# Kernel optimization log

Measured on AMD Instinct MI355X. Metric: run time of the kernel, lower is better.

The kernel has to match this reference:

```python
import jax, jax.numpy as jnp
import numpy as np

NORMALIZED_LENGTH = 512  # init kwarg
T_FRAMES = 32768
N_LM = 543  # mediapipe holistic landmark count


def setup_inputs() -> dict:
    key = jax.random.key(0)
    kf, kn, kd, ki = jax.random.split(key, 4)
    frames = jax.random.uniform(kf, (T_FRAMES, N_LM, 3), dtype=jnp.float32)
    nan_mask = jax.random.uniform(kn, (T_FRAMES, N_LM, 3)) < 0.10
    frames = jnp.where(nan_mask, jnp.float32(jnp.nan), frames)
    drop = jax.random.uniform(kd, (T_FRAMES,)) < 0.05
    hand_zone = jnp.arange(N_LM) >= 468
    frames = jnp.where(drop[:, None, None] & hand_zone[None, :, None], jnp.float32(jnp.nan), frames)
    lips_idx = jax.random.randint(ki, (40,), 0, 468, dtype=jnp.int32)
    return {"frames": frames, "lips_idx": lips_idx}


def _nan_mean0(x):
    # tf_nan_mean over axis 0 (keepdims); 0/0 -> NaN in TF is immediately zeroed
    # afterwards, so we emit 0 directly (identical forward values, safe grads).
    finite = ~jnp.isnan(x)
    s = jnp.where(finite, x, jnp.zeros((), x.dtype)).sum(axis=0, keepdims=True)
    c = finite.sum(axis=0, keepdims=True)
    return jnp.where(c == 0, jnp.zeros((), x.dtype), s / jnp.maximum(c, 1).astype(x.dtype))


def reference(frames, lips_idx):
    fr = frames[:, :, :2]                       # drop z coord
    lh = fr[:, 468:489]                         # [T, 21, 2]
    rh = fr[:, 522:543]                         # [T, 21, 2]
    lh = jnp.stack([lh[..., 0], 1.0 - lh[..., 1]], axis=-1)
    rh = jnp.stack([1.0 - rh[..., 0], 1.0 - rh[..., 1]], axis=-1)
    # stack hands, NaN->0, sum over the 2-hand axis
    hand = jnp.nan_to_num(lh) + jnp.nan_to_num(rh)   # [T, 21, 2]
    keep = hand.sum(axis=(1, 2)) != 0.0              # frames with >=1 visible hand
    hand = hand[keep]                                # [S, 21, 2]
    lips = fr[:, lips_idx][keep]                     # [S, 40, 2]
    lips = jnp.where(jnp.isnan(lips), _nan_mean0(lips), lips)
    raw = jnp.concatenate([hand, lips], axis=1)      # [S, 61, 2]
    S = int(raw.shape[0])
    # tf.linspace(0, S-1, L+1) cast to int32 -> segment boundaries (truncation)
    b = np.linspace(0.0, S - 1.0, NORMALIZED_LENGTH + 1).astype(np.int32)
    # frame t belongs to bin i with b[i] <= t < b[i+1]; t >= b[L] maps to L (dropped)
    seg = jnp.asarray(np.searchsorted(b, np.arange(S), side="right") - 1)
    sums = jax.ops.segment_sum(raw, seg, num_segments=NORMALIZED_LENGTH)
    cnt = jax.ops.segment_sum(jnp.ones((S,), raw.dtype), seg, num_segments=NORMALIZED_LENGTH)
    # raw is NaN-free at this point, so nan-mean == plain mean; empty bin -> NaN -> 0
    mean = jnp.where(cnt[:, None, None] == 0, jnp.zeros((), raw.dtype),
                     sums / jnp.maximum(cnt, 1.0)[:, None, None])
    sampled = mean.reshape(NORMALIZED_LENGTH, -1)    # Flatten -> [L, 122]
    rows = sampled.sum(axis=1) != 0.0                # drop all-zero (empty) bins
    return sampled[rows]
```

## Files before the change

kernel.cpp:

```cpp
#include <hip/hip_runtime.h>

#define T_FRAMES 32768
#define ROWF 1629
#define NSEG 512
#define NVAL 122
#define STRIDE 128
#define PADI 16

__global__ __launch_bounds__(1024) void k1_keep_stats(
    const float* __restrict__ frames, const int* __restrict__ lips_idx,
    int* __restrict__ keep, float* __restrict__ lip_sum,
    int* __restrict__ lip_cnt, float* __restrict__ stage) {
  __shared__ float ls[80];
  __shared__ int lc[80];
  int tid = threadIdx.x;
  if (tid < 80) { ls[tid] = 0.0f; lc[tid] = 0; }
  __syncthreads();

  int lane = tid & 63;
  int wid = tid >> 6;
  int t = blockIdx.x * 16 + wid;
  const float* f = frames + (size_t)t * ROWF;
  float* srow = stage + (size_t)t * STRIDE;

  float hv = 0.0f;
  if (lane < 42) {
    int j = lane >> 1, c = lane & 1;
    float lh = f[(468 + j) * 3 + c];
    float rh = f[(522 + j) * 3 + c];
    float a = (c == 0) ? lh : (1.0f - lh);
    float b = 1.0f - rh;
    a = (a == a) ? a : 0.0f;
    b = (b == b) ? b : 0.0f;
    hv = a + b;
    srow[lane] = hv;
  }
  float s = hv;
  #pragma unroll
  for (int off = 32; off > 0; off >>= 1) s += __shfl_down(s, off);
  s = __shfl(s, 0);
  int kp = (s != 0.0f) ? 1 : 0;
  if (lane == 0) keep[t] = kp;

  #pragma unroll
  for (int p = 0; p < 2; ++p) {
    int v = lane + p * 64;
    if (v < 80) {
      int j = v >> 1, c = v & 1;
      float x = f[lips_idx[j] * 3 + c];
      srow[42 + v] = x;
      if (kp && (x == x)) {
        atomicAdd(&ls[v], x);
        atomicAdd(&lc[v], 1);
      }
    }
  }
  __syncthreads();
  if (tid < 80) {
    atomicAdd(&lip_sum[tid * PADI], ls[tid]);
    atomicAdd(&lip_cnt[tid * PADI], lc[tid]);
  }
}

__global__ __launch_bounds__(1024) void k2_scan(const int* __restrict__ keep,
                                                int* __restrict__ kept_t,
                                                int* __restrict__ Sp) {
  __shared__ int wsum[16];
  int tid = threadIdx.x;
  const int PER = T_FRAMES / 1024;
  int base = tid * PER;
  int fl[PER];
  int local = 0;
  #pragma unroll
  for (int k = 0; k < PER; ++k) { fl[k] = keep[base + k]; local += fl[k]; }

  int lane = tid & 63, wid = tid >> 6;
  int scan = local;
  #pragma unroll
  for (int off = 1; off < 64; off <<= 1) {
    int n = __shfl_up(scan, off);
    if (lane >= off) scan += n;
  }
  if (lane == 63) wsum[wid] = scan;
  __syncthreads();
  if (tid < 16) {
    int v = wsum[tid];
    #pragma unroll
    for (int off = 1; off < 16; off <<= 1) {
      int n = __shfl_up(v, off);
      if (tid >= off) v += n;
    }
    wsum[tid] = v;
  }
  __syncthreads();
  int excl = ((wid == 0) ? 0 : wsum[wid - 1]) + (scan - local);
  #pragma unroll
  for (int k = 0; k < PER; ++k) {
    if (fl[k]) kept_t[excl++] = base + k;
  }
  if (tid == 1023) Sp[0] = wsum[15];
}

__global__ __launch_bounds__(512) void k3_segments(
    const float* __restrict__ stage, const int* __restrict__ kept_t,
    const int* __restrict__ Sp, const float* __restrict__ lip_sum,
    const int* __restrict__ lip_cnt, float* __restrict__ out, int out_size) {
  __shared__ int seglist[128];
  __shared__ float part[4][128];
  int tid = threadIdx.x;
  int v = tid & 127;
  int r = tid >> 7;
  int seg = blockIdx.x;
  long long Sm1 = (long long)Sp[0] - 1;
  if (Sm1 < 0) Sm1 = 0;
  int lo = (int)(((long long)seg * Sm1) >> 9);
  int hi = (int)(((long long)(seg + 1) * Sm1) >> 9);
  int cnt = hi - lo;

  for (int k = tid; k < cnt; k += 512) seglist[k] = kept_t[lo + k];
  __syncthreads();

  float cm = 0.0f;
  if (v >= 42 && v < NVAL) {
    int w = v - 42;
    int c = lip_cnt[w * PADI];
    cm = (c == 0) ? 0.0f : lip_sum[w * PADI] / (float)c;
  }

  float acc = 0.0f;
  if (v < NVAL) {
    for (int k = r; k < cnt; k += 4) {
      float x = stage[(size_t)seglist[k] * STRIDE + v];
      acc += (x == x) ? x : cm;
    }
  }
  part[r][v] = acc;
  __syncthreads();
  if (r == 0 && v < NVAL) {
    float tot = part[0][v] + part[1][v] + part[2][v] + part[3][v];
    float mean = (cnt == 0) ? 0.0f : tot / (float)cnt;
    int o = seg * NVAL + v;
    if (o < out_size) out[o] = mean;
  }
}

extern "C" void kernel_launch(void* const* d_in, const int* in_sizes, int n_in,
                              void* d_out, int out_size, void* d_ws, size_t ws_size,
                              hipStream_t stream) {
  const float* frames = (const float*)d_in[0];
  const int* lips_idx = (const int*)d_in[1];
  float* out = (float*)d_out;

  char* ws = (char*)d_ws;
  int* keep      = (int*)(ws);
  int* kept_t    = (int*)(ws + 131072);
  int* Sp        = (int*)(ws + 262144);
  float* lip_sum = (float*)(ws + 262208);
  int* lip_cnt   = (int*)(ws + 267328);
  float* stage   = (float*)(ws + 274432);

  hipMemsetAsync((void*)lip_sum, 0, 10240, stream);

  k1_keep_stats<<<2048, 1024, 0, stream>>>(frames, lips_idx, keep, lip_sum,
                                           lip_cnt, stage);
  k2_scan<<<1, 1024, 0, stream>>>(keep, kept_t, Sp);
  k3_segments<<<NSEG, 512, 0, stream>>>(stage, kept_t, Sp, lip_sum, lip_cnt,
                                        out, out_size);
}
```

Baseline: 320.4 us.

## Fuse compaction scan into stats kernel via last-block pattern; skip dropped frames

```diff
diff --git a/kernel.cpp b/kernel.cpp
--- a/kernel.cpp
+++ b/kernel.cpp
@@ -6,20 +6,25 @@
 #define NVAL 122
 #define STRIDE 128
 #define PADI 16
+#define K1_BLOCKS 2048
 
-__global__ __launch_bounds__(1024) void k1_keep_stats(
+__global__ __launch_bounds__(1024) void k1_fused(
     const float* __restrict__ frames, const int* __restrict__ lips_idx,
     int* __restrict__ keep, float* __restrict__ lip_sum,
-    int* __restrict__ lip_cnt, float* __restrict__ stage) {
+    int* __restrict__ lip_cnt, float* __restrict__ stage,
+    int* __restrict__ counter, int* __restrict__ kept_t,
+    int* __restrict__ Sp) {
   __shared__ float ls[80];
   __shared__ int lc[80];
+  __shared__ int wsum[16];
+  __shared__ int isLast;
   int tid = threadIdx.x;
   if (tid < 80) { ls[tid] = 0.0f; lc[tid] = 0; }
   __syncthreads();
 
   int lane = tid & 63;
-  int wid = tid >> 6;
-  int t = blockIdx.x * 16 + wid;
+  int wv = tid >> 6;
+  int t = blockIdx.x * 16 + wv;
   const float* f = frames + (size_t)t * ROWF;
   float* srow = stage + (size_t)t * STRIDE;
 
@@ -33,7 +38,6 @@
     a = (a == a) ? a : 0.0f;
     b = (b == b) ? b : 0.0f;
     hv = a + b;
-    srow[lane] = hv;
   }
   float s = hv;
   #pragma unroll
@@ -42,16 +46,19 @@
   int kp = (s != 0.0f) ? 1 : 0;
   if (lane == 0) keep[t] = kp;
 
-  #pragma unroll
-  for (int p = 0; p < 2; ++p) {
-    int v = lane + p * 64;
-    if (v < 80) {
-      int j = v >> 1, c = v & 1;
-      float x = f[lips_idx[j] * 3 + c];
-      srow[42 + v] = x;
-      if (kp && (x == x)) {
-        atomicAdd(&ls[v], x);
-        atomicAdd(&lc[v], 1);
+  if (kp) {
+    if (lane < 42) srow[lane] = hv;
+    #pragma unroll
+    for (int p = 0; p < 2; ++p) {
+      int v = lane + p * 64;
+      if (v < 80) {
+        int j = v >> 1, c = v & 1;
+        float x = f[lips_idx[j] * 3 + c];
+        srow[42 + v] = x;
+        if (x == x) {
+          atomicAdd(&ls[v], x);
+          atomicAdd(&lc[v], 1);
+        }
       }
     }
   }
@@ -60,28 +67,30 @@
     atomicAdd(&lip_sum[tid * PADI], ls[tid]);
     atomicAdd(&lip_cnt[tid * PADI], lc[tid]);
   }
-}
 
-__global__ __launch_bounds__(1024) void k2_scan(const int* __restrict__ keep,
-                                                int* __restrict__ kept_t,
-                                                int* __restrict__ Sp) {
-  __shared__ int wsum[16];
-  int tid = threadIdx.x;
+  __syncthreads();
+  if (tid == 0) {
+    __threadfence();
+    int prev = atomicAdd(counter, 1);
+    isLast = (prev == K1_BLOCKS - 1) ? 1 : 0;
+  }
+  __syncthreads();
+  if (!isLast) return;
+  __threadfence();
+
   const int PER = T_FRAMES / 1024;
   int base = tid * PER;
-  int fl[PER];
   int local = 0;
-  #pragma unroll
-  for (int k = 0; k < PER; ++k) { fl[k] = keep[base + k]; local += fl[k]; }
+  #pragma unroll 8
+  for (int k = 0; k < PER; ++k) local += keep[base + k];
 
-  int lane = tid & 63, wid = tid >> 6;
   int scan = local;
   #pragma unroll
   for (int off = 1; off < 64; off <<= 1) {
     int n = __shfl_up(scan, off);
     if (lane >= off) scan += n;
   }
-  if (lane == 63) wsum[wid] = scan;
+  if (lane == 63) wsum[wv] = scan;
   __syncthreads();
   if (tid < 16) {
     int v = wsum[tid];
@@ -93,10 +102,9 @@
     wsum[tid] = v;
   }
   __syncthreads();
-  int excl = ((wid == 0) ? 0 : wsum[wid - 1]) + (scan - local);
-  #pragma unroll
+  int excl = ((wv == 0) ? 0 : wsum[wv - 1]) + (scan - local);
   for (int k = 0; k < PER; ++k) {
-    if (fl[k]) kept_t[excl++] = base + k;
+    if (keep[base + k]) kept_t[excl++] = base + k;
   }
   if (tid == 1023) Sp[0] = wsum[15];
 }
@@ -155,15 +163,15 @@
   int* keep      = (int*)(ws);
   int* kept_t    = (int*)(ws + 131072);
   int* Sp        = (int*)(ws + 262144);
+  int* counter   = (int*)(ws + 262144 + 4);
   float* lip_sum = (float*)(ws + 262208);
   int* lip_cnt   = (int*)(ws + 267328);
   float* stage   = (float*)(ws + 274432);
 
-  hipMemsetAsync((void*)lip_sum, 0, 10240, stream);
+  hipMemsetAsync((void*)(ws + 262144), 0, 12288, stream);
 
-  k1_keep_stats<<<2048, 1024, 0, stream>>>(frames, lips_idx, keep, lip_sum,
-                                           lip_cnt, stage);
-  k2_scan<<<1, 1024, 0, stream>>>(keep, kept_t, Sp);
+  k1_fused<<<K1_BLOCKS, 1024, 0, stream>>>(frames, lips_idx, keep, lip_sum,
+                                           lip_cnt, stage, counter, kept_t, Sp);
   k3_segments<<<NSEG, 512, 0, stream>>>(stage, kept_t, Sp, lip_sum, lip_cnt,
                                         out, out_size);
 }
```

Result: slower. 427.6 us (+33.5%).

## Stage frame groups into LDS with vector loads and replace global atomics with partials

Applied to the files above, without the earlier changes.

```diff
diff --git a/kernel.cpp b/kernel.cpp
--- a/kernel.cpp
+++ b/kernel.cpp
@@ -5,68 +5,97 @@
 #define NSEG 512
 #define NVAL 122
 #define STRIDE 128
-#define PADI 16
+#define G 8
+#define NBLK (T_FRAMES / G)
 
-__global__ __launch_bounds__(1024) void k1_keep_stats(
+__global__ __launch_bounds__(1024) void k1_stream(
     const float* __restrict__ frames, const int* __restrict__ lips_idx,
-    int* __restrict__ keep, float* __restrict__ lip_sum,
-    int* __restrict__ lip_cnt, float* __restrict__ stage) {
+    int* __restrict__ keep, float* __restrict__ psum, int* __restrict__ pcnt,
+    float* __restrict__ stage) {
+  __shared__ float buf[G * ROWF];
   __shared__ float ls[80];
   __shared__ int lc[80];
+  __shared__ int idx3[40];
   int tid = threadIdx.x;
   if (tid < 80) { ls[tid] = 0.0f; lc[tid] = 0; }
+  if (tid < 40) idx3[tid] = lips_idx[tid] * 3;
+
+  const float4* src = (const float4*)(frames + (size_t)blockIdx.x * (G * ROWF));
+  float4* dst = (float4*)buf;
+  #pragma unroll
+  for (int i = tid; i < (G * ROWF) / 4; i += 1024) dst[i] = src[i];
   __syncthreads();
 
   int lane = tid & 63;
-  int wid = tid >> 6;
-  int t = blockIdx.x * 16 + wid;
-  const float* f = frames + (size_t)t * ROWF;
-  float* srow = stage + (size_t)t * STRIDE;
+  int wv = tid >> 6;
+  if (wv < G) {
+    const float* fb = buf + wv * ROWF;
+    int t = blockIdx.x * G + wv;
+    float* srow = stage + (size_t)t * STRIDE;
 
-  float hv = 0.0f;
-  if (lane < 42) {
-    int j = lane >> 1, c = lane & 1;
-    float lh = f[(468 + j) * 3 + c];
-    float rh = f[(522 + j) * 3 + c];
-    float a = (c == 0) ? lh : (1.0f - lh);
-    float b = 1.0f - rh;
-    a = (a == a) ? a : 0.0f;
-    b = (b == b) ? b : 0.0f;
-    hv = a + b;
-    srow[lane] = hv;
-  }
-  float s = hv;
-  #pragma unroll
-  for (int off = 32; off > 0; off >>= 1) s += __shfl_down(s, off);
-  s = __shfl(s, 0);
-  int kp = (s != 0.0f) ? 1 : 0;
-  if (lane == 0) keep[t] = kp;
+    float hv = 0.0f;
+    if (lane < 42) {
+      int j = lane >> 1, c = lane & 1;
+      float lh = fb[1404 + 3 * j + c];
+      float rh = fb[1566 + 3 * j + c];
+      float a = (c == 0) ? lh : (1.0f - lh);
+      float b = 1.0f - rh;
+      a = (a == a) ? a : 0.0f;
+      b = (b == b) ? b : 0.0f;
+      hv = a + b;
+      srow[lane] = hv;
+    }
+    float s = hv;
+    #pragma unroll
+    for (int off = 32; off > 0; off >>= 1) s += __shfl_down(s, off);
+    s = __shfl(s, 0);
+    int kp = (s != 0.0f) ? 1 : 0;
+    if (lane == 0) keep[t] = kp;
 
-  #pragma unroll
-  for (int p = 0; p < 2; ++p) {
-    int v = lane + p * 64;
-    if (v < 80) {
-      int j = v >> 1, c = v & 1;
-      float x = f[lips_idx[j] * 3 + c];
-      srow[42 + v] = x;
-      if (kp && (x == x)) {
-        atomicAdd(&ls[v], x);
-        atomicAdd(&lc[v], 1);
+    #pragma unroll
+    for (int p = 0; p < 2; ++p) {
+      int v = lane + p * 64;
+      if (v < 80) {
+        int j = v >> 1, c = v & 1;
+        float x = fb[idx3[j] + c];
+        srow[42 + v] = x;
+        if (kp && (x == x)) {
+          atomicAdd(&ls[v], x);
+          atomicAdd(&lc[v], 1);
+        }
       }
     }
   }
   __syncthreads();
   if (tid < 80) {
-    atomicAdd(&lip_sum[tid * PADI], ls[tid]);
-    atomicAdd(&lip_cnt[tid * PADI], lc[tid]);
+    psum[(size_t)tid * NBLK + blockIdx.x] = ls[tid];
+    pcnt[(size_t)tid * NBLK + blockIdx.x] = lc[tid];
   }
 }
 
-__global__ __launch_bounds__(1024) void k2_scan(const int* __restrict__ keep,
-                                                int* __restrict__ kept_t,
-                                                int* __restrict__ Sp) {
+__global__ __launch_bounds__(1024) void k2_scan(
+    const int* __restrict__ keep, int* __restrict__ kept_t,
+    int* __restrict__ Sp, const float* __restrict__ psum,
+    const int* __restrict__ pcnt, float* __restrict__ lip_sum,
+    int* __restrict__ lip_cnt) {
   __shared__ int wsum[16];
   int tid = threadIdx.x;
+  int lane = tid & 63, wv = tid >> 6;
+
+  for (int col = wv; col < 80; col += 16) {
+    float s = 0.0f; int c = 0;
+    for (int b = lane; b < NBLK; b += 64) {
+      s += psum[(size_t)col * NBLK + b];
+      c += pcnt[(size_t)col * NBLK + b];
+    }
+    #pragma unroll
+    for (int off = 32; off > 0; off >>= 1) {
+      s += __shfl_down(s, off);
+      c += __shfl_down(c, off);
+    }
+    if (lane == 0) { lip_sum[col] = s; lip_cnt[col] = c; }
+  }
+
   const int PER = T_FRAMES / 1024;
   int base = tid * PER;
   int fl[PER];
@@ -74,14 +103,13 @@
   #pragma unroll
   for (int k = 0; k < PER; ++k) { fl[k] = keep[base + k]; local += fl[k]; }
 
-  int lane = tid & 63, wid = tid >> 6;
   int scan = local;
   #pragma unroll
   for (int off = 1; off < 64; off <<= 1) {
     int n = __shfl_up(scan, off);
     if (lane >= off) scan += n;
   }
-  if (lane == 63) wsum[wid] = scan;
+  if (lane == 63) wsum[wv] = scan;
   __syncthreads();
   if (tid < 16) {
     int v = wsum[tid];
@@ -93,7 +121,7 @@
     wsum[tid] = v;
   }
   __syncthreads();
-  int excl = ((wid == 0) ? 0 : wsum[wid - 1]) + (scan - local);
+  int excl = ((wv == 0) ? 0 : wsum[wv - 1]) + (scan - local);
   #pragma unroll
   for (int k = 0; k < PER; ++k) {
     if (fl[k]) kept_t[excl++] = base + k;
@@ -123,8 +151,8 @@
   float cm = 0.0f;
   if (v >= 42 && v < NVAL) {
     int w = v - 42;
-    int c = lip_cnt[w * PADI];
-    cm = (c == 0) ? 0.0f : lip_sum[w * PADI] / (float)c;
+    int c = lip_cnt[w];
+    cm = (c == 0) ? 0.0f : lip_sum[w] / (float)c;
   }
 
   float acc = 0.0f;
@@ -156,14 +184,16 @@
   int* kept_t    = (int*)(ws + 131072);
   int* Sp        = (int*)(ws + 262144);
   float* lip_sum = (float*)(ws + 262208);
-  int* lip_cnt   = (int*)(ws + 267328);
-  float* stage   = (float*)(ws + 274432);
+  int* lip_cnt   = (int*)(ws + 262720);
+  float* psum    = (float*)(ws + 263232);
+  int* pcnt      = (int*)(ws + 1573952);
+  float* stage   = (float*)(ws + 2884672);
 
-  hipMemsetAsync((void*)lip_sum, 0, 10240, stream);
 
-  k1_keep_stats<<<2048, 1024, 0, stream>>>(frames, lips_idx, keep, lip_sum,
-                                           lip_cnt, stage);
-  k2_scan<<<1, 1024, 0, stream>>>(keep, kept_t, Sp);
+  k1_stream<<<NBLK, 1024, 0, stream>>>(frames, lips_idx, keep, psum, pcnt,
+                                       stage);
+  k2_scan<<<1, 1024, 0, stream>>>(keep, kept_t, Sp, psum, pcnt, lip_sum,
+                                  lip_cnt);
   k3_segments<<<NSEG, 512, 0, stream>>>(stage, kept_t, Sp, lip_sum, lip_cnt,
                                         out, out_size);
 }
```

Result: slower. 410.1 us (+28.0%).
